# Optimization experiments

Measured on AMD Instinct MI355X. Metric: run time of the kernel, lower is better.

Reference implementation:

```python
import jax, jax.numpy as jnp
import numpy as np

B, L = 4, 8192
IN_CH, OUT_CH = 1, 1
H = 64               # d_model
NSTATE = 16          # d_state
DBLK = 4             # number of residual blocks
DCONV = 16
EXPAND = 2
DINNER = EXPAND * H              # 128
HEADDIM = H // 4                 # 16
NHEADS = DINNER // HEADDIM       # 8
CONV_DIM = DINNER + 2 * NSTATE   # 160 (ngroups=1)
D_IN_PROJ = 2 * DINNER + 2 * NSTATE + NHEADS  # 296
CHUNK = 128


def setup_inputs():
    key = jax.random.key(0)
    ks = jax.random.split(key, 12)
    rn = lambda k, shape, s: (jax.random.normal(k, shape) * s).astype(jnp.float32)
    x = rn(ks[0], (B, L, IN_CH), 1.0)
    w_in = rn(ks[1], (H, IN_CH), 1.0)
    w_out = rn(ks[2], (OUT_CH, H), 1.0 / np.sqrt(H))
    in_proj_w = rn(ks[3], (DBLK, D_IN_PROJ, H), 1.0 / np.sqrt(H))
    conv_w = rn(ks[4], (DBLK, CONV_DIM, DCONV), 1.0 / np.sqrt(DCONV))
    conv_b = rn(ks[5], (DBLK, CONV_DIM), 0.02)
    dt = jnp.exp(jax.random.uniform(ks[6], (DBLK, NHEADS)) * (np.log(0.1) - np.log(1e-3)) + np.log(1e-3))
    dt_bias = (dt + jnp.log(-jnp.expm1(-dt))).astype(jnp.float32)  # inverse softplus
    A_log = jnp.log(jax.random.uniform(ks[7], (DBLK, NHEADS), minval=1.0, maxval=16.0)).astype(jnp.float32)
    D_skip = jnp.ones((DBLK, NHEADS), jnp.float32)
    init_states = rn(ks[8], (DBLK, NHEADS, HEADDIM, NSTATE), 0.01)
    norm_w = jnp.ones((DBLK, DINNER), jnp.float32)
    out_proj_w = rn(ks[9], (DBLK, H, DINNER), 1.0 / np.sqrt(DINNER))
    mlp_w = rn(ks[10], (DBLK, H, H), 1.0 / np.sqrt(H))
    mlp_b = jnp.zeros((DBLK, H), jnp.float32)
    return {"x": x, "w_in": w_in, "w_out": w_out, "in_proj_w": in_proj_w,
            "conv_w": conv_w, "conv_b": conv_b, "dt_bias": dt_bias, "A_log": A_log,
            "D_skip": D_skip, "init_states": init_states, "norm_w": norm_w,
            "out_proj_w": out_proj_w, "mlp_w": mlp_w, "mlp_b": mlp_b}


def segsum(a):
    # a: (..., q) -> (..., q, q); seg[i, j] = sum_{k=j+1..i} a[k] on lower triangle (diag=0), exp->0 above
    q = a.shape[-1]
    cs = jnp.cumsum(a, axis=-1)
    seg = cs[..., :, None] - cs[..., None, :]
    mask = jnp.tril(jnp.ones((q, q), dtype=bool))
    return jnp.where(mask, seg, -1e30)


def ssd(X, dA, Bm, Cm, init_state):
    # Chunked SSD (Mamba2 paper). X: (b,l,h,p) = x*dt, dA: (b,l,h), Bm/Cm: (b,l,n), init_state: (b,h,p,n)
    b, l, h, p = X.shape
    c = l // CHUNK
    X = X.reshape(b, c, CHUNK, h, p)
    Bm = Bm.reshape(b, c, CHUNK, NSTATE)
    Cm = Cm.reshape(b, c, CHUNK, NSTATE)
    A = dA.reshape(b, c, CHUNK, h).transpose(0, 3, 1, 2)  # (b,h,c,q)
    A_cs = jnp.cumsum(A, axis=-1)
    # intra-chunk (diagonal blocks)
    Lm = jnp.exp(segsum(A))  # (b,h,c,q,q)
    Y_diag = jnp.einsum('bcln,bcsn,bhcls,bcshp->bclhp', Cm, Bm, Lm, X)
    # per-chunk final states
    decay_states = jnp.exp(A_cs[..., -1:] - A_cs)  # (b,h,c,q)
    states = jnp.einsum('bcln,bhcl,bclhp->bchpn', Bm, decay_states, X)
    states = jnp.concatenate([init_state[:, None], states], axis=1)  # (b,c+1,h,p,n)
    # inter-chunk recurrence (vectorized via segsum over chunk decays)
    decay_chunk = jnp.exp(segsum(jnp.pad(A_cs[..., -1], ((0, 0), (0, 0), (1, 0)))))  # (b,h,c+1,c+1)
    new_states = jnp.einsum('bhzc,bchpn->bzhpn', decay_chunk, states)
    prev_states = new_states[:, :-1]  # state entering each chunk
    state_decay = jnp.exp(A_cs)
    Y_off = jnp.einsum('bcln,bchpn,bhcl->bclhp', Cm, prev_states, state_decay)
    return (Y_diag + Y_off).reshape(b, l, h, p)


def mamba2(u, w_inp, cw, cb, dtb, alog, dskip, istate, nw, w_outp):
    b, l, _ = u.shape
    zxbcdt = jnp.einsum('bld,ed->ble', u, w_inp)  # (b,l,296)
    z = zxbcdt[..., :DINNER]
    xBC = zxbcdt[..., DINNER:DINNER + CONV_DIM]
    dt = jax.nn.softplus(zxbcdt[..., DINNER + CONV_DIM:] + dtb)  # (b,l,h)
    # causal depthwise conv over seq + silu
    xBC = jax.lax.conv_general_dilated(
        xBC.transpose(0, 2, 1), cw[:, None, :], (1,), [(DCONV - 1, 0)],
        feature_group_count=CONV_DIM, dimension_numbers=('NCH', 'OIH', 'NCH'))
    xBC = jax.nn.silu(xBC + cb[None, :, None]).transpose(0, 2, 1)
    xs = xBC[..., :DINNER]
    Bm = xBC[..., DINNER:DINNER + NSTATE]
    Cm = xBC[..., DINNER + NSTATE:]
    A = -jnp.exp(alog)  # (h,)
    xh = xs.reshape(b, l, NHEADS, HEADDIM)
    init = jnp.broadcast_to(istate, (b,) + istate.shape)
    y = ssd(xh * dt[..., None], dt * A, Bm, Cm, init)
    y = y + xh * dskip[None, None, :, None]  # D skip
    y = y.reshape(b, l, DINNER)
    # gated RMSNorm: norm(y * silu(z)) * weight
    y = y * jax.nn.silu(z)
    y = y * jax.lax.rsqrt(jnp.mean(y * y, axis=-1, keepdims=True) + 1e-5) * nw
    return jnp.einsum('ble,de->bld', y, w_outp)


def reference(x, w_in, w_out, in_proj_w, conv_w, conv_b, dt_bias, A_log,
              D_skip, init_states, norm_w, out_proj_w, mlp_w, mlp_b):
    h = jnp.einsum('bli,hi->blh', x, w_in)
    for i in range(DBLK):
        y = mamba2(h, in_proj_w[i], conv_w[i], conv_b[i], dt_bias[i], A_log[i],
                   D_skip[i], init_states[i], norm_w[i], out_proj_w[i])
        t = y / jnp.sqrt(1.0 + y * y)  # TanhApprox
        y = jnp.einsum('blh,oh->blo', t, mlp_w[i]) + mlp_b[i]
        h = h + y  # residual
    return jnp.einsum('blh,oh->blo', h, w_out)
```

## Files before the change

kernel.cpp:

```cpp
#include <hip/hip_runtime.h>
#include <math.h>

#define NB 4
#define SEQ 8192
#define NT (NB*SEQ)
#define HDIM 64
#define NST 16
#define NBLK 4
#define KCONV 16
#define DIN 128
#define PDIM 16
#define NH 8
#define CDIM 160
#define EPROJ 296
#define CH 128
#define NC 64

typedef __attribute__((ext_vector_type(8))) short short8;
typedef __attribute__((ext_vector_type(4))) float f32x4;

__device__ __forceinline__ float sigf(float x){ return 1.0f/(1.0f+__expf(-x)); }

__device__ __forceinline__ unsigned short bf16r(float f){
  unsigned int u = __float_as_uint(f);
  u = (u + 0x7fffu + ((u >> 16) & 1u)) >> 16;
  return (unsigned short)u;
}
__device__ __forceinline__ unsigned int pk_bf16(float a, float b){
  return (unsigned int)bf16r(a) | ((unsigned int)bf16r(b) << 16);
}
__device__ __forceinline__ float bf16f(unsigned short h){
  return __uint_as_float(((unsigned int)h) << 16);
}

__global__ __launch_bounds__(256) void k_init_h(const float* __restrict__ x, const float* __restrict__ w_in,
                                                float* __restrict__ h){
  int i = blockIdx.x*256 + threadIdx.x;
  int t = i >> 6, d = i & 63;
  h[i] = x[t]*w_in[d];
}

__global__ __launch_bounds__(256) void k_wsplit(const float* __restrict__ w,
                                                unsigned short* __restrict__ whi,
                                                unsigned short* __restrict__ wlo){
  int i = blockIdx.x*256 + threadIdx.x;
  if(i < NBLK*EPROJ*HDIM){
    float f = w[i];
    unsigned short hi = bf16r(f);
    float fh = bf16f(hi);
    whi[i] = hi;
    wlo[i] = bf16r(f - fh);
  }
}

__global__ __launch_bounds__(256) void k_inproj(const float* __restrict__ h,
                                                const unsigned short* __restrict__ whi,
                                                const unsigned short* __restrict__ wlo,
                                                unsigned short* __restrict__ zxz,
                                                float* __restrict__ zxc){
  int tid = threadIdx.x;
  int lane = tid & 63, wid = tid >> 6;
  int quad = lane >> 4, lq = lane & 15;
  int t0 = blockIdx.x*64 + wid*16;

  const float* hp = h + (size_t)(t0+lq)*HDIM;
  short8 bh[2], bl[2];
#pragma unroll
  for(int kb=0;kb<2;kb++){
    float4 f0 = *(const float4*)(hp + kb*32 + quad*8);
    float4 f1 = *(const float4*)(hp + kb*32 + quad*8 + 4);
    float v[8] = {f0.x,f0.y,f0.z,f0.w,f1.x,f1.y,f1.z,f1.w};
#pragma unroll
    for(int j=0;j<8;j++){
      unsigned short hi = bf16r(v[j]);
      bh[kb][j] = (short)hi;
      bl[kb][j] = (short)bf16r(v[j] - bf16f(hi));
    }
  }

  for(int et=0; et<19; et++){
    int e_a = et*16 + lq;
    int ec = (e_a < EPROJ) ? e_a : (EPROJ-1);
    const unsigned short* wh = whi + (size_t)ec*HDIM + quad*8;
    const unsigned short* wl = wlo + (size_t)ec*HDIM + quad*8;
    short8 ah0 = *(const short8*)wh;
    short8 ah1 = *(const short8*)(wh + 32);
    short8 al0 = *(const short8*)wl;
    short8 al1 = *(const short8*)(wl + 32);
    f32x4 acc = {0.f,0.f,0.f,0.f};
    acc = __builtin_amdgcn_mfma_f32_16x16x32_bf16(ah0, bh[0], acc, 0, 0, 0);
    acc = __builtin_amdgcn_mfma_f32_16x16x32_bf16(ah1, bh[1], acc, 0, 0, 0);
    acc = __builtin_amdgcn_mfma_f32_16x16x32_bf16(ah0, bl[0], acc, 0, 0, 0);
    acc = __builtin_amdgcn_mfma_f32_16x16x32_bf16(ah1, bl[1], acc, 0, 0, 0);
    acc = __builtin_amdgcn_mfma_f32_16x16x32_bf16(al0, bh[0], acc, 0, 0, 0);
    acc = __builtin_amdgcn_mfma_f32_16x16x32_bf16(al1, bh[1], acc, 0, 0, 0);
#pragma unroll
    for(int r=0;r<4;r++){
      int e = et*16 + quad*4 + r;
      if(e < 128)        zxz[(size_t)e*NT + t0 + lq] = bf16r(acc[r]);
      else if(e < EPROJ) zxc[(size_t)(e-128)*NT + t0 + lq] = acc[r];
    }
  }
}

__global__ __launch_bounds__(512) void k_mid(const float* __restrict__ zxc,
                                             const float* __restrict__ cw, const float* __restrict__ cb,
                                             const float* __restrict__ dtb, const float* __restrict__ alog,
                                             unsigned short* __restrict__ xbc, float* __restrict__ dt,
                                             float* __restrict__ acs, float* __restrict__ asum,
                                             float* __restrict__ S){
  __shared__ unsigned short XhT[128][136];
  __shared__ unsigned short XlT[128][136];
  __shared__ unsigned short BhT[16][136];
  __shared__ unsigned short BlT[16][136];
  __shared__ float dtl[8][128];
  __shared__ float wle[8][128];

  int bc = blockIdx.x;
  int c = bc & 63, b = bc >> 6;
  int t0 = b*SEQ + c*CH;
  int tid = threadIdx.x;

  for(int it=0; it<5; it++){
    int G = tid + it*512;
    int ch = G >> 4;
    int sg = (G & 15) * 8;
    const float* p = zxc + (size_t)ch*NT + t0 + sg - 16;
    float buf[24];
    if(c == 0 && sg < 16){
#pragma unroll
      for(int j=0;j<24;j++){
        int l = sg - 16 + j;
        buf[j] = (l >= 0) ? p[j] : 0.f;
      }
    } else {
#pragma unroll
      for(int q4=0;q4<6;q4++){
        float4 f = *(const float4*)(p + q4*4);
        buf[q4*4+0]=f.x; buf[q4*4+1]=f.y; buf[q4*4+2]=f.z; buf[q4*4+3]=f.w;
      }
    }
    float wv[16];
#pragma unroll
    for(int k=0;k<16;k++) wv[k] = cw[ch*KCONV+k];
    float bias = cb[ch];
    unsigned short hs[8];
#pragma unroll
    for(int s=0;s<8;s++){
      float acc = bias;
#pragma unroll
      for(int k=0;k<16;k++) acc += wv[k]*buf[s+1+k];
      float r = acc * sigf(acc);
      unsigned short hi = bf16r(r);
      unsigned short lo = bf16r(r - bf16f(hi));
      hs[s] = hi;
      if(ch < 128){ XhT[ch][sg+s] = hi; XlT[ch][sg+s] = lo; }
      else if(ch < 144){ BhT[ch-128][sg+s] = hi; BlT[ch-128][sg+s] = lo; }
    }
    uint4 pk;
    pk.x = (unsigned int)hs[0] | ((unsigned int)hs[1] << 16);
    pk.y = (unsigned int)hs[2] | ((unsigned int)hs[3] << 16);
    pk.z = (unsigned int)hs[4] | ((unsigned int)hs[5] << 16);
    pk.w = (unsigned int)hs[6] | ((unsigned int)hs[7] << 16);
    *(uint4*)(xbc + (size_t)ch*NT + t0 + sg) = pk;
  }
#pragma unroll
  for(int k=0;k<2;k++){
    int idx = tid + k*512;
    int hh = idx >> 7, s = idx & 127;
    float raw = zxc[(size_t)(CDIM + hh)*NT + t0 + s] + dtb[hh];
    float v = (raw > 20.f) ? raw : log1pf(__expf(raw));
    dtl[hh][s] = v;
    dt[(size_t)hh*NT + t0 + s] = v;
  }
  __syncthreads();

  int lane = tid & 63, wid = tid >> 6;
  {
    int hh = wid;
    float A = -__expf(alog[hh]);
    float d0 = dtl[hh][2*lane], d1 = dtl[hh][2*lane+1];
    float v0 = d0*A, v1 = d1*A;
    float s = v0 + v1;
    for(int off=1; off<64; off<<=1){
      float o = __shfl_up(s, off);
      if(lane >= off) s += o;
    }
    float tot = __shfl(s, 63);
    float excl = s - (v0+v1);
    float a0 = excl+v0, a1 = excl+v0+v1;
    *(float2*)&acs[(size_t)hh*NT + t0 + 2*lane] = make_float2(a0, a1);
    if(lane == 63) asum[(size_t)bc*NH + hh] = tot;
    wle[hh][2*lane]   = d0*__expf(tot - a0);
    wle[hh][2*lane+1] = d1*__expf(tot - a1);
  }
  __syncthreads();

  {
    int hh = wid;
    int lq = lane & 15, quad = lane >> 4;
    f32x4 acc = {0.f,0.f,0.f,0.f};
#pragma unroll
    for(int kb=0;kb<4;kb++){
      int k0 = kb*32 + quad*8;
      short8 xh = *(const short8*)&XhT[hh*16 + lq][k0];
      short8 xl = *(const short8*)&XlT[hh*16 + lq][k0];
      short8 ah, al;
#pragma unroll
      for(int j=0;j<8;j++){
        float xv = bf16f((unsigned short)xh[j]) + bf16f((unsigned short)xl[j]);
        float pw = xv * wle[hh][k0 + j];
        unsigned short hi = bf16r(pw);
        ah[j] = (short)hi;
        al[j] = (short)bf16r(pw - bf16f(hi));
      }
      short8 bh = *(const short8*)&BhT[lq][k0];
      short8 bl = *(const short8*)&BlT[lq][k0];
      acc = __builtin_amdgcn_mfma_f32_16x16x32_bf16(ah, bh, acc, 0, 0, 0);
      acc = __builtin_amdgcn_mfma_f32_16x16x32_bf16(ah, bl, acc, 0, 0, 0);
      acc = __builtin_amdgcn_mfma_f32_16x16x32_bf16(al, bh, acc, 0, 0, 0);
    }
    float* Sp = S + ((size_t)bc*NH + hh)*256;
#pragma unroll
    for(int r=0;r<4;r++) Sp[(quad*4 + r)*16 + lq] = acc[r];
  }
}

__global__ __launch_bounds__(64) void k_scan(const float* __restrict__ S, const float* __restrict__ asum,
                                             const float* __restrict__ init, float* __restrict__ prev){
  int q  = blockIdx.x & 3;
  int hh = (blockIdx.x >> 2) & 7;
  int b  = blockIdx.x >> 5;
  int el = q*64 + threadIdx.x;
  const size_t cs = (size_t)NH*256;
  const float* Sp = S + ((size_t)(b*NC)*NH + hh)*256 + el;
  float* Pp = prev + ((size_t)(b*NC)*NH + hh)*256 + el;
  const float* ap = asum + (size_t)(b*NC)*NH + hh;
  float r = init[hh*256 + el];
  float s0 = Sp[0], s1 = Sp[cs], s2 = Sp[2*cs], s3 = Sp[3*cs];
  for(int c=0;c<NC;c+=4){
    Pp[(size_t)c*cs] = r;
    r = __expf(ap[(size_t)c*NH])*r + s0;
    s0 = (c+4 < NC) ? Sp[(size_t)(c+4)*cs] : 0.f;
    Pp[(size_t)(c+1)*cs] = r;
    r = __expf(ap[(size_t)(c+1)*NH])*r + s1;
    s1 = (c+5 < NC) ? Sp[(size_t)(c+5)*cs] : 0.f;
    Pp[(size_t)(c+2)*cs] = r;
    r = __expf(ap[(size_t)(c+2)*NH])*r + s2;
    s2 = (c+6 < NC) ? Sp[(size_t)(c+6)*cs] : 0.f;
    Pp[(size_t)(c+3)*cs] = r;
    r = __expf(ap[(size_t)(c+3)*NH])*r + s3;
    s3 = (c+7 < NC) ? Sp[(size_t)(c+7)*cs] : 0.f;
  }
}

__global__ __launch_bounds__(512) void k_tail(const unsigned short* __restrict__ xbc,
                                              const unsigned short* __restrict__ zxz,
                                              const float* __restrict__ dt, const float* __restrict__ acs,
                                              const float* __restrict__ prev, const float* __restrict__ dskip,
                                              const float* __restrict__ nw, const float* __restrict__ opw,
                                              const float* __restrict__ mw, const float* __restrict__ mb,
                                              float* __restrict__ h,
                                              int last, const float* __restrict__ wout,
                                              float* __restrict__ out){
  __shared__ __align__(16) unsigned char sm[150304];
  unsigned short* Bb   = (unsigned short*)(sm);
  unsigned short* Cb   = (unsigned short*)(sm + 6144);
  unsigned short* XbT  = (unsigned short*)(sm + 12288);
  unsigned short* P0   = (unsigned short*)(sm + 55296);
  unsigned short* P1   = (unsigned short*)(sm + 98304);
  float* Al  = (float*)(sm + 141312);
  float* Dtl = (float*)(sm + 145408);
  float* nwl = (float*)(sm + 149504);
  float* mbl = (float*)(sm + 150016);
  unsigned short* zbuf = (unsigned short*)(sm + 150272);
  unsigned short* Zb = XbT;
  unsigned short* Wo = P0;
  unsigned short* Wm = P0 + 64*136;
  unsigned short* Yn = P1;
  unsigned short* Tt = P1;

  int bc = blockIdx.x;
  int c = bc & 63, b = bc >> 6;
  int t0 = b*SEQ + c*CH;
  int tid = threadIdx.x, lane = tid & 63, wid = tid >> 6;
  int quad = lane >> 4, lq = lane & 15;

#pragma unroll
  for(int k=0;k<8;k++){
    int idx = tid + k*512;
    int ch = idx >> 7, s = idx & 127;
    unsigned short f = xbc[(size_t)(DIN+ch)*NT + t0 + s];
    if(ch < 16) Bb[s*24 + ch] = f;
    else        Cb[s*24 + ch-16] = f;
  }
#pragma unroll
  for(int k=0;k<8;k++){
    int fi = tid + k*512;
    int p = fi >> 5, s4 = fi & 31;
    uint2 xu = *(const uint2*)&xbc[(size_t)p*NT + t0 + s4*4];
    float4 dv = *(const float4*)&dt[(size_t)(p>>4)*NT + t0 + s4*4];
    float x0 = bf16f((unsigned short)(xu.x & 0xffffu));
    float x1 = bf16f((unsigned short)(xu.x >> 16));
    float x2 = bf16f((unsigned short)(xu.y & 0xffffu));
    float x3 = bf16f((unsigned short)(xu.y >> 16));
    *(unsigned int*)&XbT[p*168 + s4*4]   = pk_bf16(x0*dv.x, x1*dv.y);
    *(unsigned int*)&XbT[p*168 + s4*4+2] = pk_bf16(x2*dv.z, x3*dv.w);
  }
#pragma unroll
  for(int k=0;k<4;k++){
    int idx = tid + k*512;
    int hh = idx >> 8, rest = idx & 255;
    int p = rest >> 4, n = rest & 15;
    XbT[(hh*16+p)*168 + 128 + n] = bf16r(prev[((size_t)bc*NH + hh)*256 + rest]);
  }
#pragma unroll
  for(int k=0;k<3;k++){
    int idx = tid + k*512;
    int p = idx / 12, cc = idx - p*12;
    *(unsigned int*)&XbT[p*168 + 144 + 2*cc] = 0u;
  }
#pragma unroll
  for(int k=0;k<2;k++){
    int idx = tid + k*512;
    int hh = idx >> 7, s = idx & 127;
    Al[hh*128+s]  = acs[(size_t)hh*NT + t0 + s];
    Dtl[hh*128+s] = dt[(size_t)hh*NT + t0 + s];
  }
  if(tid < 128) nwl[tid] = nw[tid];
  else if(tid < 192) mbl[tid-128] = mb[tid-128];
  else if(tid < 208) zbuf[tid-192] = 0;
  __syncthreads();

  int strip = wid*16;
#pragma unroll
  for(int k=0;k<3;k++){
    int idx = lane + k*64;
    int rr = idx / 12, cc = idx - rr*12;
    *(unsigned int*)&P0[(strip+rr)*168 + 144 + 2*cc] = 0u;
    *(unsigned int*)&P1[(strip+rr)*168 + 144 + 2*cc] = 0u;
  }

  short8 afr;
  {
    int row = strip + lq;
    const unsigned short* ap = (quad < 2) ? &Cb[row*24 + quad*8] : zbuf;
    afr = *(const short8*)ap;
  }
  f32x4 sc[8];
#pragma unroll
  for(int nt=0;nt<8;nt++){
    const unsigned short* bp = (quad < 2) ? &Bb[(nt*16+lq)*24 + quad*8] : zbuf;
    short8 bfr = *(const short8*)bp;
    f32x4 acc = {0.f,0.f,0.f,0.f};
    sc[nt] = __builtin_amdgcn_mfma_f32_16x16x32_bf16(afr, bfr, acc, 0, 0, 0);
  }

  f32x4 accv[8];
  {
    const float* Alh = Al;
    unsigned short* Pb = P0;
    float alr[4];
#pragma unroll
    for(int r=0;r<4;r++) alr[r] = Alh[strip + quad*4 + r];
#pragma unroll
    for(int nt=0;nt<8;nt++){
      int col = nt*16 + lq;
      float alc = Alh[col];
#pragma unroll
      for(int r=0;r<4;r++){
        int row = strip + quad*4 + r;
        float p = sc[nt][r] * __expf(alr[r] - alc);
        p = (col <= row) ? p : 0.f;
        Pb[row*168 + col] = bf16r(p);
      }
    }
    int n = lane & 15, rg = lane >> 4;
#pragma unroll
    for(int rr=0;rr<4;rr++){
      int row = strip + rg*4 + rr;
      float ea = __expf(Alh[row]);
      Pb[row*168 + 128 + n] = bf16r(bf16f(Cb[row*24+n]) * ea);
    }
  }
  for(int hh2=0; hh2<8; hh2++){
    if(hh2 < 7){
      const float* Alh = Al + (hh2+1)*128;
      unsigned short* Pb = ((hh2+1)&1) ? P1 : P0;
      float alr[4];
#pragma unroll
      for(int r=0;r<4;r++) alr[r] = Alh[strip + quad*4 + r];
#pragma unroll
      for(int nt=0;nt<8;nt++){
        int col = nt*16 + lq;
        float alc = Alh[col];
#pragma unroll
        for(int r=0;r<4;r++){
          int row = strip + quad*4 + r;
          float p = sc[nt][r] * __expf(alr[r] - alc);
          p = (col <= row) ? p : 0.f;
          Pb[row*168 + col] = bf16r(p);
        }
      }
      int n = lane & 15, rg = lane >> 4;
#pragma unroll
      for(int rr=0;rr<4;rr++){
        int row = strip + rg*4 + rr;
        float ea = __expf(Alh[row]);
        Pb[row*168 + 128 + n] = bf16r(bf16f(Cb[row*24+n]) * ea);
      }
    }
    const unsigned short* Pb = (hh2&1) ? P1 : P0;
    f32x4 acc2 = {0.f,0.f,0.f,0.f};
#pragma unroll
    for(int ks=0;ks<5;ks++){
      short8 bfr = *(const short8*)&XbT[(hh2*16+lq)*168 + ks*32 + quad*8];
      short8 af  = *(const short8*)&Pb[(strip+lq)*168 + ks*32 + quad*8];
      acc2 = __builtin_amdgcn_mfma_f32_16x16x32_bf16(af, bfr, acc2, 0, 0, 0);
    }
    const float* Dth = Dtl + hh2*128;
    float Dk = dskip[hh2];
#pragma unroll
    for(int r=0;r<4;r++){
      int l = strip + quad*4 + r;
      float xdt = bf16f(XbT[(hh2*16+lq)*168 + l]);
      float dtv = fmaxf(Dth[l], 1e-30f);
      acc2[r] += Dk * xdt * __frcp_rn(dtv);
    }
    accv[hh2] = acc2;
  }
  __syncthreads();

#pragma unroll
  for(int k=0;k<8;k++){
    int fi = tid + k*512;
    int p = fi >> 5, s4 = fi & 31;
    uint2 zu = *(const uint2*)&zxz[(size_t)p*NT + t0 + s4*4];
    *(unsigned int*)&Zb[p*136 + s4*4]   = zu.x;
    *(unsigned int*)&Zb[p*136 + s4*4+2] = zu.y;
  }
#pragma unroll
  for(int k=0;k<4;k++){
    int fi = tid + k*512;
    int n = fi >> 5, k4 = fi & 31;
    float4 wv = *(const float4*)&opw[(size_t)n*DIN + k4*4];
    *(unsigned int*)&Wo[n*136 + k4*4]   = pk_bf16(wv.x, wv.y);
    *(unsigned int*)&Wo[n*136 + k4*4+2] = pk_bf16(wv.z, wv.w);
  }
#pragma unroll
  for(int k=0;k<2;k++){
    int fi = tid + k*512;
    int n = fi >> 4, k4 = fi & 15;
    float4 wv = *(const float4*)&mw[(size_t)n*HDIM + k4*4];
    *(unsigned int*)&Wm[n*72 + k4*4]   = pk_bf16(wv.x, wv.y);
    *(unsigned int*)&Wm[n*72 + k4*4+2] = pk_bf16(wv.z, wv.w);
  }
  __syncthreads();

  float rms_[4];
#pragma unroll
  for(int r=0;r<4;r++){
    int l = strip + quad*4 + r;
    float part = 0.f;
#pragma unroll
    for(int hh2=0;hh2<8;hh2++){
      float zv = bf16f(Zb[(hh2*16+lq)*136 + l]);
      float g = zv * sigf(zv);
      float yv = accv[hh2][r] * g;
      accv[hh2][r] = yv;
      part += yv*yv;
    }
    part += __shfl_xor(part,1); part += __shfl_xor(part,2);
    part += __shfl_xor(part,4); part += __shfl_xor(part,8);
    rms_[r] = rsqrtf(part*(1.0f/128.0f) + 1e-5f);
  }
#pragma unroll
  for(int hh2=0;hh2<8;hh2++){
    float nwv = nwl[hh2*16+lq];
#pragma unroll
    for(int r=0;r<4;r++){
      int l = strip + quad*4 + r;
      Yn[l*136 + hh2*16+lq] = bf16r(accv[hh2][r]*rms_[r]*nwv);
    }
  }

  short8 afk[4];
#pragma unroll
  for(int ks=0;ks<4;ks++) afk[ks] = *(const short8*)&Yn[(strip+lq)*136 + ks*32 + quad*8];
  f32x4 aco[4];
#pragma unroll
  for(int nt=0;nt<4;nt++){ aco[nt] = (f32x4){0.f,0.f,0.f,0.f}; }
#pragma unroll
  for(int nt=0;nt<4;nt++){
#pragma unroll
    for(int ks=0;ks<4;ks++){
      short8 bfr = *(const short8*)&Wo[(nt*16+lq)*136 + ks*32 + quad*8];
      aco[nt] = __builtin_amdgcn_mfma_f32_16x16x32_bf16(afk[ks], bfr, aco[nt], 0, 0, 0);
    }
  }

#pragma unroll
  for(int nt=0;nt<4;nt++){
#pragma unroll
    for(int r=0;r<4;r++){
      int l = strip + quad*4 + r;
      float o = aco[nt][r];
      Tt[l*136 + nt*16+lq] = bf16r(o * rsqrtf(1.0f + o*o));
    }
  }

  f32x4 acm[4];
#pragma unroll
  for(int nt=0;nt<4;nt++){ acm[nt] = (f32x4){0.f,0.f,0.f,0.f}; }
#pragma unroll
  for(int ks=0;ks<2;ks++){
    short8 af = *(const short8*)&Tt[(strip+lq)*136 + ks*32 + quad*8];
#pragma unroll
    for(int nt=0;nt<4;nt++){
      short8 bfr = *(const short8*)&Wm[(nt*16+lq)*72 + ks*32 + quad*8];
      acm[nt] = __builtin_amdgcn_mfma_f32_16x16x32_bf16(af, bfr, acm[nt], 0, 0, 0);
    }
  }
  if(!last){
#pragma unroll
    for(int nt=0;nt<4;nt++){
#pragma unroll
      for(int r=0;r<4;r++){
        int l = strip + quad*4 + r;
        int d = nt*16 + lq;
        size_t gi = (size_t)(t0+l)*HDIM + d;
        h[gi] += acm[nt][r] + mbl[d];
      }
    }
  } else {
    float ps[4] = {0.f,0.f,0.f,0.f};
#pragma unroll
    for(int nt=0;nt<4;nt++){
      int d = nt*16 + lq;
      float wo = wout[d];
      float bias = mbl[d];
#pragma unroll
      for(int r=0;r<4;r++){
        int l = strip + quad*4 + r;
        size_t gi = (size_t)(t0+l)*HDIM + d;
        float hn = h[gi] + acm[nt][r] + bias;
        ps[r] += hn * wo;
      }
    }
#pragma unroll
    for(int r=0;r<4;r++){
      ps[r] += __shfl_xor(ps[r],1); ps[r] += __shfl_xor(ps[r],2);
      ps[r] += __shfl_xor(ps[r],4); ps[r] += __shfl_xor(ps[r],8);
    }
    if(lq == 0){
#pragma unroll
      for(int r=0;r<4;r++) out[t0 + strip + quad*4 + r] = ps[r];
    }
  }
}

extern "C" void kernel_launch(void* const* d_in, const int* in_sizes, int n_in,
                              void* d_out, int out_size, void* d_ws, size_t ws_size,
                              hipStream_t stream){
  const float* x          = (const float*)d_in[0];
  const float* w_in       = (const float*)d_in[1];
  const float* w_out      = (const float*)d_in[2];
  const float* in_proj_w  = (const float*)d_in[3];
  const float* conv_w     = (const float*)d_in[4];
  const float* conv_b     = (const float*)d_in[5];
  const float* dt_bias    = (const float*)d_in[6];
  const float* A_log      = (const float*)d_in[7];
  const float* D_skip     = (const float*)d_in[8];
  const float* init_st    = (const float*)d_in[9];
  const float* norm_w     = (const float*)d_in[10];
  const float* out_proj_w = (const float*)d_in[11];
  const float* mlp_w      = (const float*)d_in[12];
  const float* mlp_b      = (const float*)d_in[13];
  float* out = (float*)d_out;

  float* ws = (float*)d_ws;
  float* h    = ws; ws += (size_t)NT*HDIM;
  unsigned short* zxz = (unsigned short*)ws; ws += (size_t)(128*NT)/2;
  float* zxc  = ws; ws += (size_t)168*NT;
  unsigned short* xbc = (unsigned short*)ws; ws += (size_t)(CDIM*NT)/2;
  float* dt   = ws; ws += (size_t)NH*NT;
  float* acs  = ws; ws += (size_t)NH*NT;
  float* asum = ws; ws += (size_t)NB*NC*NH;
  float* S    = ws; ws += (size_t)NB*NC*NH*256;
  float* prev = ws; ws += (size_t)NB*NC*NH*256;
  unsigned short* whi = (unsigned short*)ws; ws += (size_t)(NBLK*EPROJ*HDIM)/2;
  unsigned short* wlo = (unsigned short*)ws; ws += (size_t)(NBLK*EPROJ*HDIM)/2;

  k_init_h<<<(NT*HDIM)/256, 256, 0, stream>>>(x, w_in, h);
  k_wsplit<<<(NBLK*EPROJ*HDIM + 255)/256, 256, 0, stream>>>(in_proj_w, whi, wlo);
  for(int i=0;i<NBLK;i++){
    k_inproj<<<NT/64, 256, 0, stream>>>(h, whi + (size_t)i*EPROJ*HDIM,
                                        wlo + (size_t)i*EPROJ*HDIM, zxz, zxc);
    k_mid   <<<NB*NC, 512, 0, stream>>>(zxc, conv_w + i*CDIM*KCONV, conv_b + i*CDIM,
                                        dt_bias + i*NH, A_log + i*NH,
                                        xbc, dt, acs, asum, S);
    k_scan  <<<NB*NH*4, 64, 0, stream>>>(S, asum, init_st + i*NH*256, prev);
    k_tail  <<<NB*NC, 512, 0, stream>>>(xbc, zxz, dt, acs, prev, D_skip + i*NH,
                                        norm_w + i*DIN, out_proj_w + i*HDIM*DIN,
                                        mlp_w + i*HDIM*HDIM, mlp_b + i*HDIM, h,
                                        (i == NBLK-1) ? 1 : 0, w_out, out);
  }
}
```

Measured before the change: 370.3 us.

## Split k_tail heads across two 512-thread halves with 1024-thread blocks

Doubles the k_tail block to 1024 threads. Each half of the waves handles four of the eight heads in its own P buffer, instead of one wave group looping over all heads with double buffering. The RMSNorm sum is combined across the halves through shared memory, and the out-projection and MLP output tiles are split between the halves. The aim is more waves per block to hide latency on a grid of only 256 blocks, at the cost of extra barriers, a little more LDS, and tighter register limits under the 1024-thread launch bound.

Result: no change. 363.7 us (-1.8%).

```diff
diff --git a/kernel.cpp b/kernel.cpp
--- a/kernel.cpp
+++ b/kernel.cpp
@@ -254,16 +254,16 @@
   }
 }
 
-__global__ __launch_bounds__(512) void k_tail(const unsigned short* __restrict__ xbc,
-                                              const unsigned short* __restrict__ zxz,
-                                              const float* __restrict__ dt, const float* __restrict__ acs,
-                                              const float* __restrict__ prev, const float* __restrict__ dskip,
-                                              const float* __restrict__ nw, const float* __restrict__ opw,
-                                              const float* __restrict__ mw, const float* __restrict__ mb,
-                                              float* __restrict__ h,
-                                              int last, const float* __restrict__ wout,
-                                              float* __restrict__ out){
-  __shared__ __align__(16) unsigned char sm[150304];
+__global__ __launch_bounds__(1024) void k_tail(const unsigned short* __restrict__ xbc,
+                                               const unsigned short* __restrict__ zxz,
+                                               const float* __restrict__ dt, const float* __restrict__ acs,
+                                               const float* __restrict__ prev, const float* __restrict__ dskip,
+                                               const float* __restrict__ nw, const float* __restrict__ opw,
+                                               const float* __restrict__ mw, const float* __restrict__ mb,
+                                               float* __restrict__ h,
+                                               int last, const float* __restrict__ wout,
+                                               float* __restrict__ out){
+  __shared__ __align__(16) unsigned char sm[151840];
   unsigned short* Bb   = (unsigned short*)(sm);
   unsigned short* Cb   = (unsigned short*)(sm + 6144);
   unsigned short* XbT  = (unsigned short*)(sm + 12288);
@@ -274,6 +274,8 @@
   float* nwl = (float*)(sm + 149504);
   float* mbl = (float*)(sm + 150016);
   unsigned short* zbuf = (unsigned short*)(sm + 150272);
+  float* ssl  = (float*)(sm + 150304);
+  float* outb = (float*)(sm + 151328);
   unsigned short* Zb = XbT;
   unsigned short* Wo = P0;
   unsigned short* Wm = P0 + 64*136;
@@ -285,18 +287,20 @@
   int t0 = b*SEQ + c*CH;
   int tid = threadIdx.x, lane = tid & 63, wid = tid >> 6;
   int quad = lane >> 4, lq = lane & 15;
-
-#pragma unroll
-  for(int k=0;k<8;k++){
-    int idx = tid + k*512;
+  int hgrp = wid >> 3;
+  int strip = (wid & 7)*16;
+
+#pragma unroll
+  for(int k=0;k<4;k++){
+    int idx = tid + k*1024;
     int ch = idx >> 7, s = idx & 127;
     unsigned short f = xbc[(size_t)(DIN+ch)*NT + t0 + s];
     if(ch < 16) Bb[s*24 + ch] = f;
     else        Cb[s*24 + ch-16] = f;
   }
 #pragma unroll
-  for(int k=0;k<8;k++){
-    int fi = tid + k*512;
+  for(int k=0;k<4;k++){
+    int fi = tid + k*1024;
     int p = fi >> 5, s4 = fi & 31;
     uint2 xu = *(const uint2*)&xbc[(size_t)p*NT + t0 + s4*4];
     float4 dv = *(const float4*)&dt[(size_t)(p>>4)*NT + t0 + s4*4];
@@ -308,38 +312,38 @@
     *(unsigned int*)&XbT[p*168 + s4*4+2] = pk_bf16(x2*dv.z, x3*dv.w);
   }
 #pragma unroll
-  for(int k=0;k<4;k++){
-    int idx = tid + k*512;
+  for(int k=0;k<2;k++){
+    int idx = tid + k*1024;
     int hh = idx >> 8, rest = idx & 255;
     int p = rest >> 4, n = rest & 15;
     XbT[(hh*16+p)*168 + 128 + n] = bf16r(prev[((size_t)bc*NH + hh)*256 + rest]);
   }
 #pragma unroll
-  for(int k=0;k<3;k++){
-    int idx = tid + k*512;
-    int p = idx / 12, cc = idx - p*12;
-    *(unsigned int*)&XbT[p*168 + 144 + 2*cc] = 0u;
-  }
-#pragma unroll
   for(int k=0;k<2;k++){
-    int idx = tid + k*512;
-    int hh = idx >> 7, s = idx & 127;
+    int idx = tid + k*1024;
+    if(idx < 1536){
+      int p = idx / 12, cc = idx - p*12;
+      *(unsigned int*)&XbT[p*168 + 144 + 2*cc] = 0u;
+    }
+  }
+  {
+    int hh = tid >> 7, s = tid & 127;
     Al[hh*128+s]  = acs[(size_t)hh*NT + t0 + s];
     Dtl[hh*128+s] = dt[(size_t)hh*NT + t0 + s];
   }
   if(tid < 128) nwl[tid] = nw[tid];
   else if(tid < 192) mbl[tid-128] = mb[tid-128];
   else if(tid < 208) zbuf[tid-192] = 0;
-  __syncthreads();
-
-  int strip = wid*16;
-#pragma unroll
-  for(int k=0;k<3;k++){
-    int idx = lane + k*64;
-    int rr = idx / 12, cc = idx - rr*12;
-    *(unsigned int*)&P0[(strip+rr)*168 + 144 + 2*cc] = 0u;
-    *(unsigned int*)&P1[(strip+rr)*168 + 144 + 2*cc] = 0u;
-  }
+  {
+    unsigned short* Pg = hgrp ? P1 : P0;
+#pragma unroll
+    for(int k=0;k<3;k++){
+      int idx = lane + k*64;
+      int rr = idx / 12, cc = idx - rr*12;
+      *(unsigned int*)&Pg[(strip+rr)*168 + 144 + 2*cc] = 0u;
+    }
+  }
+  __syncthreads();
 
   short8 afr;
   {
@@ -356,10 +360,11 @@
     sc[nt] = __builtin_amdgcn_mfma_f32_16x16x32_bf16(afr, bfr, acc, 0, 0, 0);
   }
 
-  f32x4 accv[8];
-  {
-    const float* Alh = Al;
-    unsigned short* Pb = P0;
+  unsigned short* Pg = hgrp ? P1 : P0;
+  f32x4 accv[4];
+  for(int j=0;j<4;j++){
+    int hh2 = hgrp*4 + j;
+    const float* Alh = Al + hh2*128;
     float alr[4];
 #pragma unroll
     for(int r=0;r<4;r++) alr[r] = Alh[strip + quad*4 + r];
@@ -372,50 +377,23 @@
         int row = strip + quad*4 + r;
         float p = sc[nt][r] * __expf(alr[r] - alc);
         p = (col <= row) ? p : 0.f;
-        Pb[row*168 + col] = bf16r(p);
-      }
-    }
-    int n = lane & 15, rg = lane >> 4;
-#pragma unroll
-    for(int rr=0;rr<4;rr++){
-      int row = strip + rg*4 + rr;
-      float ea = __expf(Alh[row]);
-      Pb[row*168 + 128 + n] = bf16r(bf16f(Cb[row*24+n]) * ea);
-    }
-  }
-  for(int hh2=0; hh2<8; hh2++){
-    if(hh2 < 7){
-      const float* Alh = Al + (hh2+1)*128;
-      unsigned short* Pb = ((hh2+1)&1) ? P1 : P0;
-      float alr[4];
-#pragma unroll
-      for(int r=0;r<4;r++) alr[r] = Alh[strip + quad*4 + r];
-#pragma unroll
-      for(int nt=0;nt<8;nt++){
-        int col = nt*16 + lq;
-        float alc = Alh[col];
-#pragma unroll
-        for(int r=0;r<4;r++){
-          int row = strip + quad*4 + r;
-          float p = sc[nt][r] * __expf(alr[r] - alc);
-          p = (col <= row) ? p : 0.f;
-          Pb[row*168 + col] = bf16r(p);
-        }
-      }
+        Pg[row*168 + col] = bf16r(p);
+      }
+    }
+    {
       int n = lane & 15, rg = lane >> 4;
 #pragma unroll
       for(int rr=0;rr<4;rr++){
         int row = strip + rg*4 + rr;
         float ea = __expf(Alh[row]);
-        Pb[row*168 + 128 + n] = bf16r(bf16f(Cb[row*24+n]) * ea);
-      }
-    }
-    const unsigned short* Pb = (hh2&1) ? P1 : P0;
+        Pg[row*168 + 128 + n] = bf16r(bf16f(Cb[row*24+n]) * ea);
+      }
+    }
     f32x4 acc2 = {0.f,0.f,0.f,0.f};
 #pragma unroll
     for(int ks=0;ks<5;ks++){
       short8 bfr = *(const short8*)&XbT[(hh2*16+lq)*168 + ks*32 + quad*8];
-      short8 af  = *(const short8*)&Pb[(strip+lq)*168 + ks*32 + quad*8];
+      short8 af  = *(const short8*)&Pg[(strip+lq)*168 + ks*32 + quad*8];
       acc2 = __builtin_amdgcn_mfma_f32_16x16x32_bf16(af, bfr, acc2, 0, 0, 0);
     }
     const float* Dth = Dtl + hh2*128;
@@ -427,29 +405,28 @@
       float dtv = fmaxf(Dth[l], 1e-30f);
       acc2[r] += Dk * xdt * __frcp_rn(dtv);
     }
-    accv[hh2] = acc2;
-  }
-  __syncthreads();
-
-#pragma unroll
-  for(int k=0;k<8;k++){
-    int fi = tid + k*512;
+    accv[j] = acc2;
+  }
+  __syncthreads();
+
+#pragma unroll
+  for(int k=0;k<4;k++){
+    int fi = tid + k*1024;
     int p = fi >> 5, s4 = fi & 31;
     uint2 zu = *(const uint2*)&zxz[(size_t)p*NT + t0 + s4*4];
     *(unsigned int*)&Zb[p*136 + s4*4]   = zu.x;
     *(unsigned int*)&Zb[p*136 + s4*4+2] = zu.y;
   }
 #pragma unroll
-  for(int k=0;k<4;k++){
-    int fi = tid + k*512;
+  for(int k=0;k<2;k++){
+    int fi = tid + k*1024;
     int n = fi >> 5, k4 = fi & 31;
     float4 wv = *(const float4*)&opw[(size_t)n*DIN + k4*4];
     *(unsigned int*)&Wo[n*136 + k4*4]   = pk_bf16(wv.x, wv.y);
     *(unsigned int*)&Wo[n*136 + k4*4+2] = pk_bf16(wv.z, wv.w);
   }
-#pragma unroll
-  for(int k=0;k<2;k++){
-    int fi = tid + k*512;
+  {
+    int fi = tid;
     int n = fi >> 4, k4 = fi & 15;
     float4 wv = *(const float4*)&mw[(size_t)n*HDIM + k4*4];
     *(unsigned int*)&Wm[n*72 + k4*4]   = pk_bf16(wv.x, wv.y);
@@ -457,85 +434,96 @@
   }
   __syncthreads();
 
+  float part[4] = {0.f,0.f,0.f,0.f};
+#pragma unroll
+  for(int j=0;j<4;j++){
+    int ch = (hgrp*4+j)*16 + lq;
+    float nwv = nwl[ch];
+#pragma unroll
+    for(int r=0;r<4;r++){
+      int l = strip + quad*4 + r;
+      float zv = bf16f(Zb[ch*136 + l]);
+      float g = zv * sigf(zv);
+      float yv = accv[j][r] * g;
+      part[r] += yv*yv;
+      Yn[l*136 + ch] = bf16r(yv * nwv);
+    }
+  }
+#pragma unroll
+  for(int r=0;r<4;r++){
+    part[r] += __shfl_xor(part[r],1); part[r] += __shfl_xor(part[r],2);
+    part[r] += __shfl_xor(part[r],4); part[r] += __shfl_xor(part[r],8);
+  }
+  if(lq == 0){
+#pragma unroll
+    for(int r=0;r<4;r++) ssl[hgrp*128 + strip + quad*4 + r] = part[r];
+  }
+  __syncthreads();
+
   float rms_[4];
 #pragma unroll
   for(int r=0;r<4;r++){
     int l = strip + quad*4 + r;
-    float part = 0.f;
-#pragma unroll
-    for(int hh2=0;hh2<8;hh2++){
-      float zv = bf16f(Zb[(hh2*16+lq)*136 + l]);
-      float g = zv * sigf(zv);
-      float yv = accv[hh2][r] * g;
-      accv[hh2][r] = yv;
-      part += yv*yv;
-    }
-    part += __shfl_xor(part,1); part += __shfl_xor(part,2);
-    part += __shfl_xor(part,4); part += __shfl_xor(part,8);
-    rms_[r] = rsqrtf(part*(1.0f/128.0f) + 1e-5f);
-  }
-#pragma unroll
-  for(int hh2=0;hh2<8;hh2++){
-    float nwv = nwl[hh2*16+lq];
+    rms_[r] = rsqrtf((ssl[l] + ssl[128+l])*(1.0f/128.0f) + 1e-5f);
+  }
+  short8 afk[4];
+#pragma unroll
+  for(int ks=0;ks<4;ks++) afk[ks] = *(const short8*)&Yn[(strip+lq)*136 + ks*32 + quad*8];
+  f32x4 aco[2];
+#pragma unroll
+  for(int ntl=0;ntl<2;ntl++){ aco[ntl] = (f32x4){0.f,0.f,0.f,0.f}; }
+#pragma unroll
+  for(int ntl=0;ntl<2;ntl++){
+    int nt = hgrp*2 + ntl;
+#pragma unroll
+    for(int ks=0;ks<4;ks++){
+      short8 bfr = *(const short8*)&Wo[(nt*16+lq)*136 + ks*32 + quad*8];
+      aco[ntl] = __builtin_amdgcn_mfma_f32_16x16x32_bf16(afk[ks], bfr, aco[ntl], 0, 0, 0);
+    }
+  }
+  __syncthreads();
+#pragma unroll
+  for(int ntl=0;ntl<2;ntl++){
+    int nt = hgrp*2 + ntl;
 #pragma unroll
     for(int r=0;r<4;r++){
       int l = strip + quad*4 + r;
-      Yn[l*136 + hh2*16+lq] = bf16r(accv[hh2][r]*rms_[r]*nwv);
-    }
-  }
-
-  short8 afk[4];
-#pragma unroll
-  for(int ks=0;ks<4;ks++) afk[ks] = *(const short8*)&Yn[(strip+lq)*136 + ks*32 + quad*8];
-  f32x4 aco[4];
-#pragma unroll
-  for(int nt=0;nt<4;nt++){ aco[nt] = (f32x4){0.f,0.f,0.f,0.f}; }
-#pragma unroll
-  for(int nt=0;nt<4;nt++){
-#pragma unroll
-    for(int ks=0;ks<4;ks++){
-      short8 bfr = *(const short8*)&Wo[(nt*16+lq)*136 + ks*32 + quad*8];
-      aco[nt] = __builtin_amdgcn_mfma_f32_16x16x32_bf16(afk[ks], bfr, aco[nt], 0, 0, 0);
-    }
-  }
-
-#pragma unroll
-  for(int nt=0;nt<4;nt++){
-#pragma unroll
-    for(int r=0;r<4;r++){
-      int l = strip + quad*4 + r;
-      float o = aco[nt][r];
+      float o = aco[ntl][r] * rms_[r];
       Tt[l*136 + nt*16+lq] = bf16r(o * rsqrtf(1.0f + o*o));
     }
   }
-
-  f32x4 acm[4];
-#pragma unroll
-  for(int nt=0;nt<4;nt++){ acm[nt] = (f32x4){0.f,0.f,0.f,0.f}; }
+  __syncthreads();
+
+  f32x4 acm[2];
+#pragma unroll
+  for(int ntl=0;ntl<2;ntl++){ acm[ntl] = (f32x4){0.f,0.f,0.f,0.f}; }
 #pragma unroll
   for(int ks=0;ks<2;ks++){
     short8 af = *(const short8*)&Tt[(strip+lq)*136 + ks*32 + quad*8];
 #pragma unroll
-    for(int nt=0;nt<4;nt++){
+    for(int ntl=0;ntl<2;ntl++){
+      int nt = hgrp*2 + ntl;
       short8 bfr = *(const short8*)&Wm[(nt*16+lq)*72 + ks*32 + quad*8];
-      acm[nt] = __builtin_amdgcn_mfma_f32_16x16x32_bf16(af, bfr, acm[nt], 0, 0, 0);
+      acm[ntl] = __builtin_amdgcn_mfma_f32_16x16x32_bf16(af, bfr, acm[ntl], 0, 0, 0);
     }
   }
   if(!last){
 #pragma unroll
-    for(int nt=0;nt<4;nt++){
+    for(int ntl=0;ntl<2;ntl++){
+      int nt = hgrp*2 + ntl;
 #pragma unroll
       for(int r=0;r<4;r++){
         int l = strip + quad*4 + r;
         int d = nt*16 + lq;
         size_t gi = (size_t)(t0+l)*HDIM + d;
-        h[gi] += acm[nt][r] + mbl[d];
+        h[gi] += acm[ntl][r] + mbl[d];
       }
     }
   } else {
     float ps[4] = {0.f,0.f,0.f,0.f};
 #pragma unroll
-    for(int nt=0;nt<4;nt++){
+    for(int ntl=0;ntl<2;ntl++){
+      int nt = hgrp*2 + ntl;
       int d = nt*16 + lq;
       float wo = wout[d];
       float bias = mbl[d];
@@ -543,7 +531,7 @@
       for(int r=0;r<4;r++){
         int l = strip + quad*4 + r;
         size_t gi = (size_t)(t0+l)*HDIM + d;
-        float hn = h[gi] + acm[nt][r] + bias;
+        float hn = h[gi] + acm[ntl][r] + bias;
         ps[r] += hn * wo;
       }
     }
@@ -552,9 +540,17 @@
       ps[r] += __shfl_xor(ps[r],1); ps[r] += __shfl_xor(ps[r],2);
       ps[r] += __shfl_xor(ps[r],4); ps[r] += __shfl_xor(ps[r],8);
     }
-    if(lq == 0){
-#pragma unroll
-      for(int r=0;r<4;r++) out[t0 + strip + quad*4 + r] = ps[r];
+    if(hgrp == 1 && lq == 0){
+#pragma unroll
+      for(int r=0;r<4;r++) outb[strip + quad*4 + r] = ps[r];
+    }
+    __syncthreads();
+    if(hgrp == 0 && lq == 0){
+#pragma unroll
+      for(int r=0;r<4;r++){
+        int l = strip + quad*4 + r;
+        out[t0 + l] = ps[r] + outb[l];
+      }
     }
   }
 }
@@ -600,9 +596,9 @@
                                         dt_bias + i*NH, A_log + i*NH,
                                         xbc, dt, acs, asum, S);
     k_scan  <<<NB*NH*4, 64, 0, stream>>>(S, asum, init_st + i*NH*256, prev);
-    k_tail  <<<NB*NC, 512, 0, stream>>>(xbc, zxz, dt, acs, prev, D_skip + i*NH,
-                                        norm_w + i*DIN, out_proj_w + i*HDIM*DIN,
-                                        mlp_w + i*HDIM*HDIM, mlp_b + i*HDIM, h,
-                                        (i == NBLK-1) ? 1 : 0, w_out, out);
-  }
-}
+    k_tail  <<<NB*NC, 1024, 0, stream>>>(xbc, zxz, dt, acs, prev, D_skip + i*NH,
+                                         norm_w + i*DIN, out_proj_w + i*HDIM*DIN,
+                                         mlp_w + i*HDIM*HDIM, mlp_b + i*HDIM, h,
+                                         (i == NBLK-1) ? 1 : 0, w_out, out);
+  }
+}
```
